# Kernel tuning notes

Hardware: AMD Instinct MI355X
Metric: run time of the kernel (lower is better)

Reference implementation:

```python
import jax, jax.numpy as jnp
import numpy as np

N, E, HN, K = 4096, 8192, 1024, 8
NF, EF = 128, 64
NH = [256, 256]
EH = [64, 64]
EMB = NH[-1] + len(EH)  # 258
BN_EPS = 1e-5


def setup_inputs() -> dict:
    key = jax.random.key(0)
    ks = jax.random.split(key, 16)

    def nrm(k, shape, fan):
        return jax.random.normal(k, shape, jnp.float32) / np.float32(np.sqrt(fan))

    return {
        "X_n": jax.random.normal(ks[0], (N, NF), jnp.float32),
        "X_e": jax.random.normal(ks[1], (E, EF), jnp.float32),
        # row-normalized-ish adjacency and scaled Laplacian to keep activations bounded
        "A_tilde": jax.random.uniform(ks[2], (N, N), jnp.float32) / np.float32(N),
        "L1_tilde": jax.random.normal(ks[3], (E, E), jnp.float32) / np.float32(np.sqrt(E)),
        "B1": jax.random.normal(ks[4], (N, E), jnp.float32) / np.float32(np.sqrt(E)),
        # GNN params (Linear stores weight as [out, in])
        "gnn_W1": nrm(ks[5], (NH[0], NF), NF), "gnn_b1": jnp.zeros((NH[0],), jnp.float32),
        "gnn_W2": nrm(ks[6], (NH[1], NH[0]), NH[0]), "gnn_b2": jnp.zeros((NH[1],), jnp.float32),
        # HoSC layer 1: in=EF, out=EH[0]
        "hosc_W1": nrm(ks[7], (EH[0], EF), EF), "hosc_b1": jnp.zeros((EH[0],), jnp.float32),
        "bn1_g": jnp.ones((EH[0],), jnp.float32), "bn1_b": jnp.zeros((EH[0],), jnp.float32),
        # HoSC layer 2: in=1 (after channel-max), out=EH[1]
        "hosc_W2": nrm(ks[8], (EH[1], 1), 1), "hosc_b2": jnp.zeros((EH[1],), jnp.float32),
        "bn2_g": jnp.ones((EH[1],), jnp.float32), "bn2_b": jnp.zeros((EH[1],), jnp.float32),
        # heads
        "node_W": nrm(ks[9], (1, EMB), EMB), "node_b": jnp.zeros((1,), jnp.float32),
        "edge_W": nrm(ks[10], (1, len(EH)), len(EH)), "edge_b": jnp.zeros((1,), jnp.float32),
        "hyper_W": nrm(ks[11], (1, EMB), EMB), "hyper_b": jnp.zeros((1,), jnp.float32),
        "hyperedges": jax.random.randint(ks[12], (HN, K), 0, N, jnp.int64),
    }


def _bn(x, g, b):
    # training-mode BatchNorm1d: biased batch statistics over rows
    m = jnp.mean(x, axis=0)
    v = jnp.var(x, axis=0)
    return g * (x - m) / jnp.sqrt(v + BN_EPS) + b


def _hosc_layer(Z, L1, W, bias, g, b):
    Zt = Z @ W.T + bias            # [E, out]
    Zc = L1 @ Zt                   # [E, out]
    Zp = jax.nn.relu(_bn(Zc, g, b))
    return jnp.max(Zp, axis=1, keepdims=True)  # [E, 1]


def reference(X_n, X_e, A_tilde, L1_tilde, B1,
              gnn_W1, gnn_b1, gnn_W2, gnn_b2,
              hosc_W1, hosc_b1, bn1_g, bn1_b,
              hosc_W2, hosc_b2, bn2_g, bn2_b,
              node_W, node_b, edge_W, edge_b, hyper_W, hyper_b,
              hyperedges):
    # --- GNN over nodes ---
    H = jax.nn.relu((A_tilde @ X_n) @ gnn_W1.T + gnn_b1)   # [N, 256]
    H_n = jax.nn.relu((A_tilde @ H) @ gnn_W2.T + gnn_b2)   # [N, 256]

    # --- HoSC over edges ---
    Z1 = _hosc_layer(X_e, L1_tilde, hosc_W1, hosc_b1, bn1_g, bn1_b)  # [E, 1]
    Z2 = _hosc_layer(Z1, L1_tilde, hosc_W2, hosc_b2, bn2_g, bn2_b)   # [E, 1]
    Z_H = jnp.concatenate([Z1, Z2], axis=1)                 # [E, 2]

    # --- fuse edge info into nodes ---
    H_e = B1 @ Z_H                                          # [N, 2]
    Hcat = jnp.concatenate([H_n, H_e], axis=1)              # [N, 258]

    node_prob = jax.nn.sigmoid(Hcat @ node_W.T + node_b).squeeze(-1)  # [N]
    edge_prob = jax.nn.sigmoid(Z_H @ edge_W.T + edge_b).squeeze(-1)   # [E]

    # vectorized hyperedge gather-mean-linear-sigmoid (fixed-size hyperedges)
    hfeat = Hcat[hyperedges].mean(axis=1)                   # [HN, 258]
    hyperedge_prob = jax.nn.sigmoid(hfeat @ hyper_W.T + hyper_b)  # [HN, 1]

    return node_prob, edge_prob, hyperedge_prob, Hcat
```

## Files before the change

### kernel.cpp

```cpp
#include <hip/hip_runtime.h>
#include <hip/hip_bf16.h>

using f32x4  = __attribute__((ext_vector_type(4))) float;
using u32x4  = __attribute__((ext_vector_type(4))) unsigned int;
using bf16x8 = __attribute__((ext_vector_type(8))) short;

__device__ __forceinline__ ushort f2bf(float x) {
    union { __hip_bfloat16 h; ushort u; } cv;
    cv.h = __float2bfloat16(x);
    return cv.u;
}
__device__ __forceinline__ float sigmoidf_(float x) { return 1.f / (1.f + expf(-x)); }

template<bool SPLIT, bool RELU, bool BF16_OUT, bool HAS_BIAS>
__global__ __launch_bounds__(256)
void gemm_kernel(const float* __restrict__ A, const ushort* __restrict__ B,
                 const float* __restrict__ bias, float* __restrict__ Cf,
                 ushort* __restrict__ Cb, int M, int N, int K, int ldc, int kPerChunk)
{
    __shared__ ushort As[128 * 40];
    __shared__ ushort Bs[64 * 40];
    const int tid  = threadIdx.x;
    const int lane = tid & 63;
    const int wid  = tid >> 6;
    const int wr   = wid >> 1, wc = wid & 1;
    const int g    = lane >> 4, lr = lane & 15;
    const long m0  = (long)blockIdx.x * 128;
    const int  n0  = blockIdx.y * 64;

    int kbeg = 0, kend = K;
    if (SPLIT) { kbeg = blockIdx.z * kPerChunk; kend = kbeg + kPerChunk; if (kend > K) kend = K; }

    const int bkr = tid & 31;
    const int bcb = tid >> 5;

    f32x4 pa[4];
    u32x4 pb;
    const float* Abase = A + m0 * (long)K;

    auto loadT = [&](int k0) {
#pragma unroll
        for (int i = 0; i < 4; i++) {
            int s = tid + 256 * i; int row = s >> 3, c4 = s & 7;
            pa[i] = *(const f32x4*)(Abase + (long)row * K + k0 + c4 * 4);
        }
        pb = *(const u32x4*)(B + (long)(k0 + bkr) * N + n0 + bcb * 8);
    };
    auto storeT = [&]() {
#pragma unroll
        for (int i = 0; i < 4; i++) {
            int s = tid + 256 * i; int row = s >> 3, c4 = s & 7;
            ushort4 w;
            w.x = f2bf(pa[i].x); w.y = f2bf(pa[i].y);
            w.z = f2bf(pa[i].z); w.w = f2bf(pa[i].w);
            *(ushort4*)(&As[row * 40 + c4 * 4]) = w;
        }
        const ushort* p8 = (const ushort*)&pb;
#pragma unroll
        for (int j = 0; j < 8; j++) Bs[(bcb * 8 + j) * 40 + bkr] = p8[j];
    };

    f32x4 acc[4][2] = {};

    const int nk = (kend - kbeg) >> 5;
    loadT(kbeg);
    for (int t = 0; t < nk; ++t) {
        storeT();
        __syncthreads();
        if (t + 1 < nk) loadT(kbeg + ((t + 1) << 5));
        bf16x8 af[4], bfr[2];
#pragma unroll
        for (int fm = 0; fm < 4; fm++)
            af[fm] = *(const bf16x8*)(&As[(wr * 64 + fm * 16 + lr) * 40 + g * 8]);
#pragma unroll
        for (int fn = 0; fn < 2; fn++)
            bfr[fn] = *(const bf16x8*)(&Bs[(wc * 32 + fn * 16 + lr) * 40 + g * 8]);
#pragma unroll
        for (int fm = 0; fm < 4; fm++)
#pragma unroll
            for (int fn = 0; fn < 2; fn++)
                acc[fm][fn] = __builtin_amdgcn_mfma_f32_16x16x32_bf16(af[fm], bfr[fn], acc[fm][fn], 0, 0, 0);
        __syncthreads();
    }

    if (SPLIT) {
        float* P = Cf + (long)blockIdx.z * M * N;
#pragma unroll
        for (int fm = 0; fm < 4; fm++)
#pragma unroll
            for (int fn = 0; fn < 2; fn++)
#pragma unroll
                for (int rr = 0; rr < 4; rr++) {
                    long row = m0 + wr * 64 + fm * 16 + g * 4 + rr;
                    int  col = n0 + wc * 32 + fn * 16 + lr;
                    P[row * N + col] = acc[fm][fn][rr];
                }
    } else {
#pragma unroll
        for (int fm = 0; fm < 4; fm++)
#pragma unroll
            for (int fn = 0; fn < 2; fn++)
#pragma unroll
                for (int rr = 0; rr < 4; rr++) {
                    long row = m0 + wr * 64 + fm * 16 + g * 4 + rr;
                    int  col = n0 + wc * 32 + fn * 16 + lr;
                    float v = acc[fm][fn][rr];
                    if (HAS_BIAS) v += bias[col];
                    if (RELU) v = fmaxf(v, 0.f);
                    if (BF16_OUT) Cb[row * ldc + col] = f2bf(v);
                    else          Cf[row * ldc + col] = v;
                }
    }
}

__global__ __launch_bounds__(256) void reduce_add(const float* __restrict__ P,
                                                  float* __restrict__ C, int MN, int nz)
{
    int i = blockIdx.x * 256 + threadIdx.x;
    int n4 = MN >> 2;
    if (i >= n4) return;
    f32x4 a = ((const f32x4*)P)[i];
    for (int z = 1; z < nz; z++) a += ((const f32x4*)(P + (long)z * MN))[i];
    ((f32x4*)C)[i] = a;
}

__global__ void convert_bf16_k(const float* __restrict__ X, ushort* __restrict__ Y, int n4)
{
    int j = blockIdx.x * 256 + threadIdx.x;
    if (j >= n4) return;
    f32x4 v = ((const f32x4*)X)[j];
    ushort4 o; o.x = f2bf(v.x); o.y = f2bf(v.y); o.z = f2bf(v.z); o.w = f2bf(v.w);
    ((ushort4*)Y)[j] = o;
}

__global__ void transpose_bf16_k(const float* __restrict__ W, ushort* __restrict__ T, int O, int I)
{
    int j = blockIdx.x * 256 + threadIdx.x;
    if (j >= O * I) return;
    int i = j / O, o = j - i * O;
    T[j] = f2bf(W[(long)o * I + i]);
}

__global__ void zero_stats_k(float* stats) { if (threadIdx.x < 192) stats[threadIdx.x] = 0.f; }

__global__ __launch_bounds__(256) void bn_stats_k(const float* __restrict__ Zc,
                                                  float* __restrict__ gsum, float* __restrict__ gsq)
{
    int b = blockIdx.x, t = threadIdx.x;
    int c = t & 63, rg = t >> 6;
    float sx = 0.f, sq = 0.f;
    int base = b * 128 + rg;
#pragma unroll 8
    for (int i = 0; i < 32; i++) {
        float x = Zc[(base + 4 * i) * 64 + c];
        sx += x; sq += x * x;
    }
    __shared__ float ls[256], lq[256];
    ls[t] = sx; lq[t] = sq;
    __syncthreads();
    if (t < 64) {
        float a = ls[t] + ls[t + 64] + ls[t + 128] + ls[t + 192];
        float q = lq[t] + lq[t + 64] + lq[t + 128] + lq[t + 192];
        atomicAdd(&gsum[t], a);
        atomicAdd(&gsq[t], q);
    }
}

__global__ __launch_bounds__(256) void z1_k(const float* __restrict__ Zc,
                                            const float* __restrict__ gsum, const float* __restrict__ gsq,
                                            const float* __restrict__ g, const float* __restrict__ b,
                                            float* __restrict__ Z1)
{
    int w = threadIdx.x >> 6, lane = threadIdx.x & 63;
    int row = blockIdx.x * 4 + w;
    const float inv = 1.f / 8192.f;
    float m = gsum[lane] * inv;
    float v = gsq[lane] * inv - m * m;
    float x = Zc[row * 64 + lane];
    float y = fmaxf(g[lane] * (x - m) * rsqrtf(v + 1e-5f) + b[lane], 0.f);
#pragma unroll
    for (int o = 32; o > 0; o >>= 1) y = fmaxf(y, __shfl_xor(y, o));
    if (lane == 0) Z1[row] = y;
}

__global__ __launch_bounds__(256) void pass2_k(const float* __restrict__ L1, const float* __restrict__ Z1,
                                               float* __restrict__ s, float* __restrict__ r)
{
    int i = blockIdx.x, t = threadIdx.x;
    const f32x4* row = (const f32x4*)(L1 + (long)i * 8192);
    const f32x4* z4  = (const f32x4*)Z1;
    float as = 0.f, ar = 0.f;
#pragma unroll
    for (int k = 0; k < 8; k++) {
        f32x4 v = row[t + 256 * k];
        f32x4 z = z4[t + 256 * k];
        as += v.x * z.x + v.y * z.y + v.z * z.z + v.w * z.w;
        ar += v.x + v.y + v.z + v.w;
    }
    __shared__ float ls[256], lr[256];
    ls[t] = as; lr[t] = ar;
    __syncthreads();
    for (int off = 128; off > 0; off >>= 1) {
        if (t < off) { ls[t] += ls[t + off]; lr[t] += lr[t + off]; }
        __syncthreads();
    }
    if (t == 0) { s[i] = ls[0]; r[i] = lr[0]; }
}

__global__ __launch_bounds__(256) void stats2_k(const float* __restrict__ s, const float* __restrict__ r,
                                                float* __restrict__ S)
{
    int t = threadIdx.x;
    int i = blockIdx.x * 256 + t;
    float sv = s[i], rv = r[i];
    float vals[5] = { sv, rv, sv * sv, rv * rv, sv * rv };
    __shared__ float buf[256];
    for (int q = 0; q < 5; q++) {
        buf[t] = vals[q];
        __syncthreads();
        for (int off = 128; off > 0; off >>= 1) {
            if (t < off) buf[t] += buf[t + off];
            __syncthreads();
        }
        if (t == 0) atomicAdd(&S[q], buf[0]);
        __syncthreads();
    }
}

__global__ __launch_bounds__(256) void z2_edge_k(const float* __restrict__ s, const float* __restrict__ r,
                                                 const float* __restrict__ S,
                                                 const float* __restrict__ W2, const float* __restrict__ b2,
                                                 const float* __restrict__ g2, const float* __restrict__ bb2,
                                                 const float* __restrict__ eW, const float* __restrict__ eb,
                                                 const float* __restrict__ Z1,
                                                 float* __restrict__ Z2, float* __restrict__ edge_out)
{
    int w = threadIdx.x >> 6, lane = threadIdx.x & 63;
    int row = blockIdx.x * 4 + w;
    const float inv = 1.f / 8192.f;
    float ms = S[0] * inv, mr = S[1] * inv;
    float vs = S[2] * inv - ms * ms;
    float vr = S[3] * inv - mr * mr;
    float cv = S[4] * inv - ms * mr;
    float w2 = W2[lane], bz = b2[lane];
    float mc = w2 * ms + bz * mr;
    float vc = w2 * w2 * vs + 2.f * w2 * bz * cv + bz * bz * vr;
    float x  = w2 * s[row] + bz * r[row];
    float y  = fmaxf(g2[lane] * (x - mc) * rsqrtf(vc + 1e-5f) + bb2[lane], 0.f);
#pragma unroll
    for (int o = 32; o > 0; o >>= 1) y = fmaxf(y, __shfl_xor(y, o));
    if (lane == 0) {
        Z2[row] = y;
        float e = Z1[row] * eW[0] + y * eW[1] + eb[0];
        edge_out[row] = sigmoidf_(e);
    }
}

__global__ __launch_bounds__(256) void he_node_k(const float* __restrict__ B1, const float* __restrict__ Z1,
                                                 const float* __restrict__ Z2, float* __restrict__ hcat,
                                                 const float* __restrict__ nW, const float* __restrict__ nb,
                                                 float* __restrict__ node_out)
{
    int n = blockIdx.x, t = threadIdx.x;
    const f32x4* row = (const f32x4*)(B1 + (long)n * 8192);
    const f32x4* z1v = (const f32x4*)Z1;
    const f32x4* z2v = (const f32x4*)Z2;
    float a1 = 0.f, a2 = 0.f;
#pragma unroll
    for (int k = 0; k < 8; k++) {
        f32x4 v = row[t + 256 * k];
        f32x4 p = z1v[t + 256 * k];
        f32x4 q = z2v[t + 256 * k];
        a1 += v.x * p.x + v.y * p.y + v.z * p.z + v.w * p.w;
        a2 += v.x * q.x + v.y * q.y + v.z * q.z + v.w * q.w;
    }
    __shared__ float l1s[256], l2s[256];
    __shared__ float hv[2];
    l1s[t] = a1; l2s[t] = a2;
    __syncthreads();
    for (int off = 128; off > 0; off >>= 1) {
        if (t < off) { l1s[t] += l1s[t + off]; l2s[t] += l2s[t + off]; }
        __syncthreads();
    }
    if (t == 0) {
        hcat[(long)n * 258 + 256] = l1s[0];
        hcat[(long)n * 258 + 257] = l2s[0];
        hv[0] = l1s[0]; hv[1] = l2s[0];
    }
    __syncthreads();
    float d = hcat[(long)n * 258 + t] * nW[t];
    l1s[t] = d;
    __syncthreads();
    for (int off = 128; off > 0; off >>= 1) {
        if (t < off) l1s[t] += l1s[t + off];
        __syncthreads();
    }
    if (t == 0) {
        float tot = l1s[0] + hv[0] * nW[256] + hv[1] * nW[257] + nb[0];
        node_out[n] = sigmoidf_(tot);
    }
}

__global__ __launch_bounds__(256) void hyper_k(const void* __restrict__ he_idx,
                                               const float* __restrict__ hcat,
                                               const float* __restrict__ hW, const float* __restrict__ hb,
                                               float* __restrict__ out)
{
    int w = threadIdx.x >> 6, lane = threadIdx.x & 63;
    int h = blockIdx.x * 4 + w;
    const unsigned int* u = (const unsigned int*)he_idx;
    unsigned int odd = u[2 * lane + 1];
    bool is64 = __all(odd == 0u);
    float acc = 0.f;
    for (int k = 0; k < 8; k++) {
        int idx;
        if (is64) idx = (int)((const long long*)he_idx)[h * 8 + k];
        else      idx = ((const int*)he_idx)[h * 8 + k];
        const float* hr = hcat + (long)idx * 258;
        for (int d = lane; d < 258; d += 64) acc += hr[d] * hW[d];
    }
    acc *= 0.125f;
#pragma unroll
    for (int o = 32; o > 0; o >>= 1) acc += __shfl_xor(acc, o);
    if (lane == 0) out[h] = sigmoidf_(acc + hb[0]);
}

extern "C" void kernel_launch(void* const* d_in, const int* in_sizes, int n_in,
                              void* d_out, int out_size, void* d_ws, size_t ws_size,
                              hipStream_t stream)
{
    const float* X_n  = (const float*)d_in[0];
    const float* X_e  = (const float*)d_in[1];
    const float* A_t  = (const float*)d_in[2];
    const float* L1   = (const float*)d_in[3];
    const float* B1   = (const float*)d_in[4];
    const float* gW1  = (const float*)d_in[5];
    const float* gb1  = (const float*)d_in[6];
    const float* gW2  = (const float*)d_in[7];
    const float* gb2  = (const float*)d_in[8];
    const float* hW1  = (const float*)d_in[9];
    const float* hb1  = (const float*)d_in[10];
    const float* bn1g = (const float*)d_in[11];
    const float* bn1b = (const float*)d_in[12];
    const float* hW2  = (const float*)d_in[13];
    const float* hb2  = (const float*)d_in[14];
    const float* bn2g = (const float*)d_in[15];
    const float* bn2b = (const float*)d_in[16];
    const float* nW   = (const float*)d_in[17];
    const float* nb   = (const float*)d_in[18];
    const float* eW   = (const float*)d_in[19];
    const float* ebb  = (const float*)d_in[20];
    const float* yW   = (const float*)d_in[21];
    const float* yb   = (const float*)d_in[22];
    const void*  he   = d_in[23];

    float* out       = (float*)d_out;
    float* out_node  = out;
    float* out_edge  = out + 4096;
    float* out_hyper = out + 12288;
    float* hcat      = out + 13312;

    size_t off = 0;
    auto alloc = [&](size_t bytes) {
        void* p = (char*)d_ws + off;
        off = (off + bytes + 255) & ~(size_t)255;
        return p;
    };
    ushort* Xn_bf = (ushort*)alloc(4096 * 128 * 2);
    ushort* W1t   = (ushort*)alloc(128 * 256 * 2);
    ushort* W2t   = (ushort*)alloc(256 * 256 * 2);
    ushort* W1ht  = (ushort*)alloc(64 * 64 * 2);
    float*  C1    = (float*)alloc(4096 * 128 * 4);
    ushort* H_bf  = (ushort*)alloc(4096 * 256 * 2);
    float*  C2    = (float*)alloc(4096 * 256 * 4);
    ushort* Zt1   = (ushort*)alloc(8192 * 64 * 2);
    float*  Zc1   = (float*)alloc(8192 * 64 * 4);
    float*  stats = (float*)alloc(256 * 4);
    float*  gsum  = stats;
    float*  gsq   = stats + 64;
    float*  S5    = stats + 128;
    float*  Z1    = (float*)alloc(8192 * 4);
    float*  Z2    = (float*)alloc(8192 * 4);
    float*  sbuf  = (float*)alloc(8192 * 4);
    float*  rbuf  = (float*)alloc(8192 * 4);
    float*  P     = (float*)alloc(2097152 * 4);

    zero_stats_k<<<1, 256, 0, stream>>>(stats);
    convert_bf16_k<<<512, 256, 0, stream>>>(X_n, Xn_bf, 4096 * 128 / 4);
    transpose_bf16_k<<<128, 256, 0, stream>>>(gW1, W1t, 256, 128);
    transpose_bf16_k<<<256, 256, 0, stream>>>(gW2, W2t, 256, 256);
    transpose_bf16_k<<<16, 256, 0, stream>>>(hW1, W1ht, 64, 64);

    gemm_kernel<true, false, false, false><<<dim3(32, 2, 4), 256, 0, stream>>>(
        A_t, Xn_bf, nullptr, P, nullptr, 4096, 128, 4096, 128, 1024);
    reduce_add<<<512, 256, 0, stream>>>(P, C1, 4096 * 128, 4);
    gemm_kernel<false, true, true, true><<<dim3(32, 4, 1), 256, 0, stream>>>(
        C1, W1t, gb1, nullptr, H_bf, 4096, 256, 128, 256, 0);
    gemm_kernel<true, false, false, false><<<dim3(32, 4, 2), 256, 0, stream>>>(
        A_t, H_bf, nullptr, P, nullptr, 4096, 256, 4096, 256, 2048);
    reduce_add<<<1024, 256, 0, stream>>>(P, C2, 4096 * 256, 2);
    gemm_kernel<false, true, false, true><<<dim3(32, 4, 1), 256, 0, stream>>>(
        C2, W2t, gb2, hcat, nullptr, 4096, 256, 256, 258, 0);

    gemm_kernel<false, false, true, true><<<dim3(64, 1, 1), 256, 0, stream>>>(
        X_e, W1ht, hb1, nullptr, Zt1, 8192, 64, 64, 64, 0);
    gemm_kernel<true, false, false, false><<<dim3(64, 1, 4), 256, 0, stream>>>(
        L1, Zt1, nullptr, P, nullptr, 8192, 64, 8192, 64, 2048);
    reduce_add<<<512, 256, 0, stream>>>(P, Zc1, 8192 * 64, 4);
    bn_stats_k<<<64, 256, 0, stream>>>(Zc1, gsum, gsq);
    z1_k<<<2048, 256, 0, stream>>>(Zc1, gsum, gsq, bn1g, bn1b, Z1);

    pass2_k<<<8192, 256, 0, stream>>>(L1, Z1, sbuf, rbuf);
    stats2_k<<<32, 256, 0, stream>>>(sbuf, rbuf, S5);
    z2_edge_k<<<2048, 256, 0, stream>>>(sbuf, rbuf, S5, hW2, hb2, bn2g, bn2b,
                                        eW, ebb, Z1, Z2, out_edge);

    he_node_k<<<4096, 256, 0, stream>>>(B1, Z1, Z2, hcat, nW, nb, out_node);
    hyper_k<<<256, 256, 0, stream>>>(he, hcat, yW, yb, out_hyper);
}
```

Measured before the change: 304.9 us.

## Pre-convert adjacency to bf16, fuse prep/reduction kernels, use wave-per-row reductions

Converts A_tilde to bf16 once in a merged prep kernel so both large GEMMs read half the bytes and skip per-tile conversion. It also folds the small prep launches into that kernel, makes the split-K reductions emit bf16, and fuses the HoSC partial-sum reduction with the BN statistics. pass2 and he_node now use one wave per row with shuffle reductions instead of block tree reductions, and stats2 is folded into pass2 via atomics. The cost is an extra 64MB read and 32MB write of A for the conversion, plus lower precision for the C1/C2 intermediates.

```diff
diff --git a/kernel.cpp b/kernel.cpp
--- a/kernel.cpp
+++ b/kernel.cpp
@@ -10,11 +10,14 @@
     cv.h = __float2bfloat16(x);
     return cv.u;
 }
+__device__ __forceinline__ unsigned pk2(float lo, float hi) {
+    return (unsigned)f2bf(lo) | ((unsigned)f2bf(hi) << 16);
+}
 __device__ __forceinline__ float sigmoidf_(float x) { return 1.f / (1.f + expf(-x)); }
 
-template<bool SPLIT, bool RELU, bool BF16_OUT, bool HAS_BIAS>
+template<bool A_BF16, bool SPLIT, bool RELU, bool BF16_OUT, bool HAS_BIAS>
 __global__ __launch_bounds__(256)
-void gemm_kernel(const float* __restrict__ A, const ushort* __restrict__ B,
+void gemm_kernel(const void* __restrict__ Avoid, const ushort* __restrict__ B,
                  const float* __restrict__ bias, float* __restrict__ Cf,
                  ushort* __restrict__ Cb, int M, int N, int K, int ldc, int kPerChunk)
 {
@@ -34,26 +37,45 @@
     const int bkr = tid & 31;
     const int bcb = tid >> 5;
 
+    const float*  Af = (const float*)Avoid;
+    const ushort* Ab = (const ushort*)Avoid;
+
     f32x4 pa[4];
+    u32x4 pab[2];
     u32x4 pb;
-    const float* Abase = A + m0 * (long)K;
 
     auto loadT = [&](int k0) {
-#pragma unroll
-        for (int i = 0; i < 4; i++) {
-            int s = tid + 256 * i; int row = s >> 3, c4 = s & 7;
-            pa[i] = *(const f32x4*)(Abase + (long)row * K + k0 + c4 * 4);
+        if (A_BF16) {
+#pragma unroll
+            for (int i = 0; i < 2; i++) {
+                int s = tid + 256 * i; int row = s >> 2, c8 = s & 3;
+                pab[i] = *(const u32x4*)(Ab + (m0 + row) * (long)K + k0 + c8 * 8);
+            }
+        } else {
+#pragma unroll
+            for (int i = 0; i < 4; i++) {
+                int s = tid + 256 * i; int row = s >> 3, c4 = s & 7;
+                pa[i] = *(const f32x4*)(Af + (m0 + row) * (long)K + k0 + c4 * 4);
+            }
         }
         pb = *(const u32x4*)(B + (long)(k0 + bkr) * N + n0 + bcb * 8);
     };
     auto storeT = [&]() {
-#pragma unroll
-        for (int i = 0; i < 4; i++) {
-            int s = tid + 256 * i; int row = s >> 3, c4 = s & 7;
-            ushort4 w;
-            w.x = f2bf(pa[i].x); w.y = f2bf(pa[i].y);
-            w.z = f2bf(pa[i].z); w.w = f2bf(pa[i].w);
-            *(ushort4*)(&As[row * 40 + c4 * 4]) = w;
+        if (A_BF16) {
+#pragma unroll
+            for (int i = 0; i < 2; i++) {
+                int s = tid + 256 * i; int row = s >> 2, c8 = s & 3;
+                *(u32x4*)(&As[row * 40 + c8 * 8]) = pab[i];
+            }
+        } else {
+#pragma unroll
+            for (int i = 0; i < 4; i++) {
+                int s = tid + 256 * i; int row = s >> 3, c4 = s & 7;
+                ushort4 w;
+                w.x = f2bf(pa[i].x); w.y = f2bf(pa[i].y);
+                w.z = f2bf(pa[i].z); w.w = f2bf(pa[i].w);
+                *(ushort4*)(&As[row * 40 + c4 * 4]) = w;
+            }
         }
         const ushort* p8 = (const ushort*)&pb;
 #pragma unroll
@@ -113,46 +135,73 @@
     }
 }
 
-__global__ __launch_bounds__(256) void reduce_add(const float* __restrict__ P,
-                                                  float* __restrict__ C, int MN, int nz)
+__global__ __launch_bounds__(256) void reduce_add_bf16(const float* __restrict__ P,
+                                                       ushort* __restrict__ C, int MN, int nz)
 {
     int i = blockIdx.x * 256 + threadIdx.x;
     int n4 = MN >> 2;
     if (i >= n4) return;
     f32x4 a = ((const f32x4*)P)[i];
     for (int z = 1; z < nz; z++) a += ((const f32x4*)(P + (long)z * MN))[i];
-    ((f32x4*)C)[i] = a;
-}
-
-__global__ void convert_bf16_k(const float* __restrict__ X, ushort* __restrict__ Y, int n4)
-{
-    int j = blockIdx.x * 256 + threadIdx.x;
-    if (j >= n4) return;
-    f32x4 v = ((const f32x4*)X)[j];
-    ushort4 o; o.x = f2bf(v.x); o.y = f2bf(v.y); o.z = f2bf(v.z); o.w = f2bf(v.w);
-    ((ushort4*)Y)[j] = o;
-}
-
-__global__ void transpose_bf16_k(const float* __restrict__ W, ushort* __restrict__ T, int O, int I)
-{
-    int j = blockIdx.x * 256 + threadIdx.x;
-    if (j >= O * I) return;
-    int i = j / O, o = j - i * O;
-    T[j] = f2bf(W[(long)o * I + i]);
-}
-
-__global__ void zero_stats_k(float* stats) { if (threadIdx.x < 192) stats[threadIdx.x] = 0.f; }
-
-__global__ __launch_bounds__(256) void bn_stats_k(const float* __restrict__ Zc,
-                                                  float* __restrict__ gsum, float* __restrict__ gsq)
-{
+    ushort4 o; o.x = f2bf(a.x); o.y = f2bf(a.y); o.z = f2bf(a.z); o.w = f2bf(a.w);
+    ((ushort4*)C)[i] = o;
+}
+
+__global__ __launch_bounds__(256) void prep_k(const float* __restrict__ A, ushort* __restrict__ Abf,
+                                              const float* __restrict__ Xn, ushort* __restrict__ Xnb,
+                                              const float* __restrict__ W1, ushort* __restrict__ W1t,
+                                              const float* __restrict__ W2, ushort* __restrict__ W2t,
+                                              const float* __restrict__ Wh, ushort* __restrict__ Wht,
+                                              float* __restrict__ stats)
+{
+    int b = blockIdx.x, t = threadIdx.x;
+    if (b < 8192) {
+        long j = (long)b * 256 + t;
+        f32x4 v0 = ((const f32x4*)A)[2 * j];
+        f32x4 v1 = ((const f32x4*)A)[2 * j + 1];
+        u32x4 w;
+        w.x = pk2(v0.x, v0.y); w.y = pk2(v0.z, v0.w);
+        w.z = pk2(v1.x, v1.y); w.w = pk2(v1.z, v1.w);
+        ((u32x4*)Abf)[j] = w;
+    } else if (b < 8448) {
+        long j = (long)(b - 8192) * 256 + t;
+        f32x4 v0 = ((const f32x4*)Xn)[2 * j];
+        f32x4 v1 = ((const f32x4*)Xn)[2 * j + 1];
+        u32x4 w;
+        w.x = pk2(v0.x, v0.y); w.y = pk2(v0.z, v0.w);
+        w.z = pk2(v1.x, v1.y); w.w = pk2(v1.z, v1.w);
+        ((u32x4*)Xnb)[j] = w;
+    } else if (b < 8576) {
+        int j = (b - 8448) * 256 + t;
+        int i = j >> 8, o = j & 255;
+        W1t[j] = f2bf(W1[o * 128 + i]);
+    } else if (b < 8832) {
+        int j = (b - 8576) * 256 + t;
+        int i = j >> 8, o = j & 255;
+        W2t[j] = f2bf(W2[o * 256 + i]);
+    } else if (b < 8848) {
+        int j = (b - 8832) * 256 + t;
+        int i = j >> 6, o = j & 63;
+        Wht[j] = f2bf(Wh[o * 64 + i]);
+    } else {
+        if (t < 192) stats[t] = 0.f;
+    }
+}
+
+__global__ __launch_bounds__(256) void bnred_k(const float* __restrict__ P,
+                                               float* __restrict__ Zc,
+                                               float* __restrict__ gsum, float* __restrict__ gsq)
+{
+    const int MN = 8192 * 64;
     int b = blockIdx.x, t = threadIdx.x;
     int c = t & 63, rg = t >> 6;
     float sx = 0.f, sq = 0.f;
     int base = b * 128 + rg;
 #pragma unroll 8
     for (int i = 0; i < 32; i++) {
-        float x = Zc[(base + 4 * i) * 64 + c];
+        long idx = (long)(base + 4 * i) * 64 + c;
+        float x = P[idx] + P[idx + MN] + P[idx + 2 * MN] + P[idx + 3 * MN];
+        Zc[idx] = x;
         sx += x; sq += x * x;
     }
     __shared__ float ls[256], lq[256];
@@ -184,46 +233,35 @@
 }
 
 __global__ __launch_bounds__(256) void pass2_k(const float* __restrict__ L1, const float* __restrict__ Z1,
-                                               float* __restrict__ s, float* __restrict__ r)
-{
-    int i = blockIdx.x, t = threadIdx.x;
-    const f32x4* row = (const f32x4*)(L1 + (long)i * 8192);
-    const f32x4* z4  = (const f32x4*)Z1;
+                                               float* __restrict__ s, float* __restrict__ r,
+                                               float* __restrict__ S5)
+{
+    int w = threadIdx.x >> 6, l = threadIdx.x & 63;
+    int row = blockIdx.x * 4 + w;
+    const f32x4* rp = (const f32x4*)(L1 + (long)row * 8192);
+    const f32x4* z4 = (const f32x4*)Z1;
     float as = 0.f, ar = 0.f;
 #pragma unroll
-    for (int k = 0; k < 8; k++) {
-        f32x4 v = row[t + 256 * k];
-        f32x4 z = z4[t + 256 * k];
+    for (int k = 0; k < 32; k++) {
+        f32x4 v = rp[l + 64 * k];
+        f32x4 z = z4[l + 64 * k];
         as += v.x * z.x + v.y * z.y + v.z * z.z + v.w * z.w;
         ar += v.x + v.y + v.z + v.w;
     }
-    __shared__ float ls[256], lr[256];
-    ls[t] = as; lr[t] = ar;
+#pragma unroll
+    for (int o = 32; o > 0; o >>= 1) { as += __shfl_xor(as, o); ar += __shfl_xor(ar, o); }
+    __shared__ float sw[4], rw[4];
+    if (l == 0) { s[row] = as; r[row] = ar; sw[w] = as; rw[w] = ar; }
     __syncthreads();
-    for (int off = 128; off > 0; off >>= 1) {
-        if (t < off) { ls[t] += ls[t + off]; lr[t] += lr[t + off]; }
-        __syncthreads();
-    }
-    if (t == 0) { s[i] = ls[0]; r[i] = lr[0]; }
-}
-
-__global__ __launch_bounds__(256) void stats2_k(const float* __restrict__ s, const float* __restrict__ r,
-                                                float* __restrict__ S)
-{
-    int t = threadIdx.x;
-    int i = blockIdx.x * 256 + t;
-    float sv = s[i], rv = r[i];
-    float vals[5] = { sv, rv, sv * sv, rv * rv, sv * rv };
-    __shared__ float buf[256];
-    for (int q = 0; q < 5; q++) {
-        buf[t] = vals[q];
-        __syncthreads();
-        for (int off = 128; off > 0; off >>= 1) {
-            if (t < off) buf[t] += buf[t + off];
-            __syncthreads();
+    if (threadIdx.x == 0) {
+        float Ss = 0, Sr = 0, Sss = 0, Srr = 0, Ssr = 0;
+#pragma unroll
+        for (int i = 0; i < 4; i++) {
+            float sv = sw[i], rv = rw[i];
+            Ss += sv; Sr += rv; Sss += sv * sv; Srr += rv * rv; Ssr += sv * rv;
         }
-        if (t == 0) atomicAdd(&S[q], buf[0]);
-        __syncthreads();
+        atomicAdd(&S5[0], Ss); atomicAdd(&S5[1], Sr);
+        atomicAdd(&S5[2], Sss); atomicAdd(&S5[3], Srr); atomicAdd(&S5[4], Ssr);
     }
 }
 
@@ -261,44 +299,34 @@
                                                  const float* __restrict__ nW, const float* __restrict__ nb,
                                                  float* __restrict__ node_out)
 {
-    int n = blockIdx.x, t = threadIdx.x;
-    const f32x4* row = (const f32x4*)(B1 + (long)n * 8192);
+    int w = threadIdx.x >> 6, l = threadIdx.x & 63;
+    int n = blockIdx.x * 4 + w;
+    const f32x4* rp  = (const f32x4*)(B1 + (long)n * 8192);
     const f32x4* z1v = (const f32x4*)Z1;
     const f32x4* z2v = (const f32x4*)Z2;
     float a1 = 0.f, a2 = 0.f;
 #pragma unroll
-    for (int k = 0; k < 8; k++) {
-        f32x4 v = row[t + 256 * k];
-        f32x4 p = z1v[t + 256 * k];
-        f32x4 q = z2v[t + 256 * k];
+    for (int k = 0; k < 32; k++) {
+        f32x4 v = rp[l + 64 * k];
+        f32x4 p = z1v[l + 64 * k];
+        f32x4 q = z2v[l + 64 * k];
         a1 += v.x * p.x + v.y * p.y + v.z * p.z + v.w * p.w;
         a2 += v.x * q.x + v.y * q.y + v.z * q.z + v.w * q.w;
     }
-    __shared__ float l1s[256], l2s[256];
-    __shared__ float hv[2];
-    l1s[t] = a1; l2s[t] = a2;
-    __syncthreads();
-    for (int off = 128; off > 0; off >>= 1) {
-        if (t < off) { l1s[t] += l1s[t + off]; l2s[t] += l2s[t + off]; }
-        __syncthreads();
-    }
-    if (t == 0) {
-        hcat[(long)n * 258 + 256] = l1s[0];
-        hcat[(long)n * 258 + 257] = l2s[0];
-        hv[0] = l1s[0]; hv[1] = l2s[0];
-    }
-    __syncthreads();
-    float d = hcat[(long)n * 258 + t] * nW[t];
-    l1s[t] = d;
-    __syncthreads();
-    for (int off = 128; off > 0; off >>= 1) {
-        if (t < off) l1s[t] += l1s[t + off];
-        __syncthreads();
-    }
-    if (t == 0) {
-        float tot = l1s[0] + hv[0] * nW[256] + hv[1] * nW[257] + nb[0];
-        node_out[n] = sigmoidf_(tot);
-    }
+#pragma unroll
+    for (int o = 32; o > 0; o >>= 1) { a1 += __shfl_xor(a1, o); a2 += __shfl_xor(a2, o); }
+    if (l == 0) {
+        hcat[(long)n * 258 + 256] = a1;
+        hcat[(long)n * 258 + 257] = a2;
+    }
+    const float* hr = hcat + (long)n * 258;
+    float d = 0.f;
+#pragma unroll
+    for (int i = 0; i < 4; i++) d += hr[l + 64 * i] * nW[l + 64 * i];
+#pragma unroll
+    for (int o = 32; o > 0; o >>= 1) d += __shfl_xor(d, o);
+    if (l == 0)
+        node_out[n] = sigmoidf_(d + a1 * nW[256] + a2 * nW[257] + nb[0]);
 }
 
 __global__ __launch_bounds__(256) void hyper_k(const void* __restrict__ he_idx,
@@ -366,13 +394,14 @@
         off = (off + bytes + 255) & ~(size_t)255;
         return p;
     };
+    ushort* Abf   = (ushort*)alloc((size_t)4096 * 4096 * 2);
     ushort* Xn_bf = (ushort*)alloc(4096 * 128 * 2);
     ushort* W1t   = (ushort*)alloc(128 * 256 * 2);
     ushort* W2t   = (ushort*)alloc(256 * 256 * 2);
     ushort* W1ht  = (ushort*)alloc(64 * 64 * 2);
-    float*  C1    = (float*)alloc(4096 * 128 * 4);
+    ushort* C1b   = (ushort*)alloc(4096 * 128 * 2);
     ushort* H_bf  = (ushort*)alloc(4096 * 256 * 2);
-    float*  C2    = (float*)alloc(4096 * 256 * 4);
+    ushort* C2b   = (ushort*)alloc(4096 * 256 * 2);
     ushort* Zt1   = (ushort*)alloc(8192 * 64 * 2);
     float*  Zc1   = (float*)alloc(8192 * 64 * 4);
     float*  stats = (float*)alloc(256 * 4);
@@ -383,38 +412,32 @@
     float*  Z2    = (float*)alloc(8192 * 4);
     float*  sbuf  = (float*)alloc(8192 * 4);
     float*  rbuf  = (float*)alloc(8192 * 4);
-    float*  P     = (float*)alloc(2097152 * 4);
-
-    zero_stats_k<<<1, 256, 0, stream>>>(stats);
-    convert_bf16_k<<<512, 256, 0, stream>>>(X_n, Xn_bf, 4096 * 128 / 4);
-    transpose_bf16_k<<<128, 256, 0, stream>>>(gW1, W1t, 256, 128);
-    transpose_bf16_k<<<256, 256, 0, stream>>>(gW2, W2t, 256, 256);
-    transpose_bf16_k<<<16, 256, 0, stream>>>(hW1, W1ht, 64, 64);
-
-    gemm_kernel<true, false, false, false><<<dim3(32, 2, 4), 256, 0, stream>>>(
-        A_t, Xn_bf, nullptr, P, nullptr, 4096, 128, 4096, 128, 1024);
-    reduce_add<<<512, 256, 0, stream>>>(P, C1, 4096 * 128, 4);
-    gemm_kernel<false, true, true, true><<<dim3(32, 4, 1), 256, 0, stream>>>(
-        C1, W1t, gb1, nullptr, H_bf, 4096, 256, 128, 256, 0);
-    gemm_kernel<true, false, false, false><<<dim3(32, 4, 2), 256, 0, stream>>>(
-        A_t, H_bf, nullptr, P, nullptr, 4096, 256, 4096, 256, 2048);
-    reduce_add<<<1024, 256, 0, stream>>>(P, C2, 4096 * 256, 2);
-    gemm_kernel<false, true, false, true><<<dim3(32, 4, 1), 256, 0, stream>>>(
-        C2, W2t, gb2, hcat, nullptr, 4096, 256, 256, 258, 0);
-
-    gemm_kernel<false, false, true, true><<<dim3(64, 1, 1), 256, 0, stream>>>(
+    float*  P     = (float*)alloc((size_t)2097152 * 4);
+
+    prep_k<<<8849, 256, 0, stream>>>(A_t, Abf, X_n, Xn_bf, gW1, W1t, gW2, W2t, hW1, W1ht, stats);
+
+    gemm_kernel<true, true, false, false, false><<<dim3(32, 2, 4), 256, 0, stream>>>(
+        Abf, Xn_bf, nullptr, P, nullptr, 4096, 128, 4096, 128, 1024);
+    reduce_add_bf16<<<512, 256, 0, stream>>>(P, C1b, 4096 * 128, 4);
+    gemm_kernel<true, false, true, true, true><<<dim3(32, 4, 1), 256, 0, stream>>>(
+        C1b, W1t, gb1, nullptr, H_bf, 4096, 256, 128, 256, 0);
+    gemm_kernel<true, true, false, false, false><<<dim3(32, 4, 2), 256, 0, stream>>>(
+        Abf, H_bf, nullptr, P, nullptr, 4096, 256, 4096, 256, 2048);
+    reduce_add_bf16<<<1024, 256, 0, stream>>>(P, C2b, 4096 * 256, 2);
+    gemm_kernel<true, false, true, false, true><<<dim3(32, 4, 1), 256, 0, stream>>>(
+        C2b, W2t, gb2, hcat, nullptr, 4096, 256, 256, 258, 0);
+
+    gemm_kernel<false, false, false, true, true><<<dim3(64, 1, 1), 256, 0, stream>>>(
         X_e, W1ht, hb1, nullptr, Zt1, 8192, 64, 64, 64, 0);
-    gemm_kernel<true, false, false, false><<<dim3(64, 1, 4), 256, 0, stream>>>(
+    gemm_kernel<false, true, false, false, false><<<dim3(64, 1, 4), 256, 0, stream>>>(
         L1, Zt1, nullptr, P, nullptr, 8192, 64, 8192, 64, 2048);
-    reduce_add<<<512, 256, 0, stream>>>(P, Zc1, 8192 * 64, 4);
-    bn_stats_k<<<64, 256, 0, stream>>>(Zc1, gsum, gsq);
+    bnred_k<<<64, 256, 0, stream>>>(P, Zc1, gsum, gsq);
     z1_k<<<2048, 256, 0, stream>>>(Zc1, gsum, gsq, bn1g, bn1b, Z1);
 
-    pass2_k<<<8192, 256, 0, stream>>>(L1, Z1, sbuf, rbuf);
-    stats2_k<<<32, 256, 0, stream>>>(sbuf, rbuf, S5);
+    pass2_k<<<2048, 256, 0, stream>>>(L1, Z1, sbuf, rbuf, S5);
     z2_edge_k<<<2048, 256, 0, stream>>>(sbuf, rbuf, S5, hW2, hb2, bn2g, bn2b,
                                         eW, ebb, Z1, Z2, out_edge);
 
-    he_node_k<<<4096, 256, 0, stream>>>(B1, Z1, Z2, hcat, nW, nb, out_node);
+    he_node_k<<<1024, 256, 0, stream>>>(B1, Z1, Z2, hcat, nW, nb, out_node);
     hyper_k<<<256, 256, 0, stream>>>(he, hcat, yW, yb, out_hyper);
 }
```

Measured after the change: 380.4 us. 1.25x slower.
